# Kernel tuning notes

Hardware: AMD Instinct MI355X
Metric: run time of the kernel (lower is better)

## Reference

```python
import jax, jax.numpy as jnp
import numpy as np

D_MODEL = 1024
K_QUERY = 32
K_TOPK = 4

def setup_inputs() -> dict:
    key = jax.random.key(0)
    k1, k2, k3, k4, k5 = jax.random.split(key, 5)
    x = jax.random.normal(k1, (4, 2048, D_MODEL), dtype=jnp.float32)
    # nn.Linear(d_model, k_query): weight [k_query, d_model], bias [k_query]
    sc = 1.0 / np.sqrt(D_MODEL)
    Wq = jax.random.uniform(k2, (K_QUERY, D_MODEL), jnp.float32, -sc, sc)
    bq = jax.random.uniform(k3, (K_QUERY,), jnp.float32, -sc, sc)
    Wk = jax.random.uniform(k4, (K_QUERY, D_MODEL), jnp.float32, -sc, sc)
    bk = jax.random.uniform(k5, (K_QUERY,), jnp.float32, -sc, sc)
    return {"x": x, "Wq": Wq, "bq": bq, "Wk": Wk, "bk": bk}

def reference(x, Wq, bq, Wk, bk):
    # x: [B, T, D]
    queries = jnp.einsum('btd,kd->btk', x, Wq) + bq      # [B, T, Kq]
    keys = jnp.einsum('btd,kd->btk', x, Wk) + bk         # [B, T, Kq]
    sim = jnp.einsum('btk,bsk->bts', queries, keys)      # [B, T, T]
    sim = sim / jnp.sqrt(jnp.float32(queries.shape[-1]))
    _, topk_idx = jax.lax.top_k(sim, K_TOPK)              # [B, T, K]
    # gather neighbors per (b, t): x[b, topk_idx[b, t]] -> [B, T, K, D]
    neighbors = jax.vmap(lambda xb, ib: xb[ib])(x, topk_idx)
    gathered = neighbors.mean(axis=2)                     # [B, T, D]
    return gathered
```

## Files before the change

kernel.cpp:

```cpp
#include <hip/hip_runtime.h>
#include <math.h>

#define D_MODEL 1024
#define T_SEQ   2048
#define NBATCH  4
#define NROWS   (NBATCH * T_SEQ)
#define NOUT    64

#define XLD   1036
#define XLDH  1032

#define T16F   1024
#define T16DM  1025
#define T16DN  1281

typedef double v4df __attribute__((ext_vector_type(4)));
typedef float  v4f  __attribute__((ext_vector_type(4)));
typedef _Float16 v8hf __attribute__((ext_vector_type(8)));

__device__ __forceinline__ bool key_gt(float av, int ai, float bv, int bi) {
    return (av > bv) || (av == bv && ai < bi);
}

__device__ __forceinline__ void cmpswap(float& v0, int& i0, float& v1, int& i1) {
    bool sw = key_gt(v1, i1, v0, i0);
    float nv0 = sw ? v1 : v0, nv1 = sw ? v0 : v1;
    int   ni0 = sw ? i1 : i0, ni1 = sw ? i0 : i1;
    v0 = nv0; v1 = nv1; i0 = ni0; i1 = ni1;
}

__device__ __forceinline__ void merge4(float (&a)[4], int (&ai)[4],
                                       float b0, int j0, float b1, int j1,
                                       float b2, int j2, float b3, int j3) {
    if (!key_gt(a[0], ai[0], b3, j3)) { a[0] = b3; ai[0] = j3; }
    if (!key_gt(a[1], ai[1], b2, j2)) { a[1] = b2; ai[1] = j2; }
    if (!key_gt(a[2], ai[2], b1, j1)) { a[2] = b1; ai[2] = j1; }
    if (!key_gt(a[3], ai[3], b0, j0)) { a[3] = b0; ai[3] = j0; }
    cmpswap(a[0], ai[0], a[2], ai[2]);
    cmpswap(a[1], ai[1], a[3], ai[3]);
    cmpswap(a[0], ai[0], a[1], ai[1]);
    cmpswap(a[2], ai[2], a[3], ai[3]);
}

__device__ __forceinline__ void insert4(float (&tv)[4], int (&tix)[4], float v, int idx) {
    if (v > tv[3]) {
        bool g0 = v > tv[0], g1 = v > tv[1], g2 = v > tv[2];
        float n0 = g0 ? v : tv[0];
        int   m0 = g0 ? idx : tix[0];
        float n1 = g1 ? (g0 ? tv[0] : v) : tv[1];
        int   m1 = g1 ? (g0 ? tix[0] : idx) : tix[1];
        float n2 = g2 ? (g1 ? tv[1] : v) : tv[2];
        int   m2 = g2 ? (g1 ? tix[1] : idx) : tix[2];
        float n3 = g2 ? tv[2] : v;
        int   m3 = g2 ? tix[2] : idx;
        tv[0] = n0; tv[1] = n1; tv[2] = n2; tv[3] = n3;
        tix[0] = m0; tix[1] = m1; tix[2] = m2; tix[3] = m3;
    }
}

__device__ void run_probe(int tid, int* __restrict__ tab)
{
    __shared__ double Aref[16][4];
    __shared__ double Bref[4][16];
    __shared__ double Dref[16][16];

    const int lane = tid;
    if (tid < 64) {
        const int m = lane & 15, k = lane >> 4;
        Aref[m][k] = (double)(1 + m * 4 + k);
        Bref[k][m] = (double)(1 + k * 16 + m);
    }
    __syncthreads();
    {
        const int e = tid;
        const int m = e >> 4, n = e & 15;
        double s = 0.0;
        for (int k = 0; k < 4; ++k) s += Aref[m][k] * Bref[k][n];
        Dref[m][n] = s;
    }
    __syncthreads();

    if (tid >= 64) return;

    int found = -1;
    for (int h = 0; h < 16; ++h) {
        if (found >= 0) break;
        const int fa = h & 1, fb = (h >> 1) & 1, fd = h >> 2;
        const int am = fa ? (lane >> 2) : (lane & 15);
        const int ak = fa ? (lane & 3)  : (lane >> 4);
        const int bn = fb ? (lane >> 2) : (lane & 15);
        const int bk = fb ? (lane & 3)  : (lane >> 4);
        v4df c = {0.0, 0.0, 0.0, 0.0};
        c = __builtin_amdgcn_mfma_f64_16x16x4f64(Aref[am][ak], Bref[bk][bn], c, 0, 0, 0);
        bool ok = true;
        #pragma unroll
        for (int i = 0; i < 4; ++i) {
            int dm, dn;
            if (fd == 0)      { dm = 4 * (lane >> 4) + i; dn = lane & 15; }
            else if (fd == 1) { dn = 4 * (lane >> 4) + i; dm = lane & 15; }
            else if (fd == 2) { dm = (lane >> 4) + 4 * i; dn = lane & 15; }
            else              { dn = (lane >> 4) + 4 * i; dm = lane & 15; }
            if (c[i] != Dref[dm][dn]) ok = false;
        }
        if (__all(ok)) found = h;
    }

    const int fa = (found >= 0) ? (found & 1) : 0;
    const int fb = (found >= 0) ? ((found >> 1) & 1) : 0;
    const int fd = (found >= 0) ? (found >> 2) : 0;
    tab[1   + lane] = fa ? (lane >> 2) : (lane & 15);
    tab[65  + lane] = fa ? (lane & 3)  : (lane >> 4);
    tab[129 + lane] = fb ? (lane & 3)  : (lane >> 4);
    tab[193 + lane] = fb ? (lane >> 2) : (lane & 15);
    #pragma unroll
    for (int i = 0; i < 4; ++i) {
        int dm, dn;
        if (fd == 0)      { dm = 4 * (lane >> 4) + i; dn = lane & 15; }
        else if (fd == 1) { dn = 4 * (lane >> 4) + i; dm = lane & 15; }
        else if (fd == 2) { dm = (lane >> 4) + 4 * i; dn = lane & 15; }
        else              { dn = (lane >> 4) + 4 * i; dm = lane & 15; }
        tab[257 + lane * 4 + i] = dm;
        tab[513 + lane * 4 + i] = dn;
    }
    if (lane == 0) tab[0] = found;
}

__device__ void run_probe16(int tid, int* __restrict__ tab)
{
    __shared__ _Float16 A16[16][32];
    __shared__ _Float16 B16[32][16];
    __shared__ float    D16[16][16];

    for (int e = tid; e < 512; e += 256) {
        const int m = e >> 5, k = e & 31;
        A16[m][k] = (_Float16)(float)(1 + (3 * m + 5 * k) % 61);
        const int kk = e >> 4, n = e & 15;
        B16[kk][n] = (_Float16)(float)(1 + (7 * kk + 11 * n) % 59);
    }
    __syncthreads();
    {
        const int m = tid >> 4, n = tid & 15;
        float s = 0.f;
        for (int k = 0; k < 32; ++k) s += (float)A16[m][k] * (float)B16[k][n];
        D16[m][n] = s;
    }
    __syncthreads();

    if (tid >= 64) return;
    const int lane = tid;

    v8hf a, b;
    const int ab = (lane >> 4) * 8;
    #pragma unroll
    for (int j = 0; j < 8; ++j) {
        a[j] = A16[lane & 15][ab + j];
        b[j] = B16[ab + j][lane & 15];
    }
    v4f c = {0.f, 0.f, 0.f, 0.f};
    c = __builtin_amdgcn_mfma_f32_16x16x32_f16(a, b, c, 0, 0, 0);

    bool ok0 = true, ok1 = true;
    #pragma unroll
    for (int i = 0; i < 4; ++i) {
        ok0 = ok0 && (c[i] == D16[4 * (lane >> 4) + i][lane & 15]);
        ok1 = ok1 && (c[i] == D16[lane & 15][4 * (lane >> 4) + i]);
    }
    int found = __all(ok0) ? 0 : (__all(ok1) ? 1 : -1);
    const int fd = (found == 1) ? 1 : 0;
    #pragma unroll
    for (int i = 0; i < 4; ++i) {
        const int dm = fd ? (lane & 15) : (4 * (lane >> 4) + i);
        const int dn = fd ? (4 * (lane >> 4) + i) : (lane & 15);
        tab[T16DM + lane * 4 + i] = dm;
        tab[T16DN + lane * 4 + i] = dn;
    }
    if (lane == 0) tab[T16F] = found;
}

__global__ __launch_bounds__(256) void wprep_probe(
    const float* __restrict__ Wq, const float* __restrict__ Wk,
    double* __restrict__ Wdt, _Float16* __restrict__ Wh, _Float16* __restrict__ Wl,
    int* __restrict__ tab)
{
    const int tid = threadIdx.x;
    const int idx = blockIdx.x * 256 + tid;

    {
        const int o = idx & 63;
        const int d = idx >> 6;
        float v = (o < 32) ? Wq[(size_t)o * D_MODEL + d]
                           : Wk[(size_t)(o - 32) * D_MODEL + d];
        Wdt[(size_t)d * 64 + o] = (double)v;
    }
    {
        const int o = idx >> 10;
        const int d = idx & 1023;
        float v = (o < 32) ? Wq[(size_t)o * D_MODEL + d]
                           : Wk[(size_t)(o - 32) * D_MODEL + d];
        _Float16 h = (_Float16)v;
        Wh[(size_t)o * D_MODEL + d] = h;
        Wl[(size_t)o * D_MODEL + d] = (_Float16)(v - (float)h);
    }

    if (blockIdx.x == 0) {
        run_probe(tid, tab);
        run_probe16(tid, tab);
    }
}

__global__ __launch_bounds__(256) void proj(
    const float* __restrict__ x, const double* __restrict__ Wdt,
    const _Float16* __restrict__ Wh, const _Float16* __restrict__ Wl,
    const float* __restrict__ bq, const float* __restrict__ bk_,
    const int* __restrict__ tab,
    float* __restrict__ Qt, float* __restrict__ Kt)
{
    __shared__ __align__(16) char ldsraw[16 * XLD * 4];

    const int tid  = threadIdx.x;
    const int lane = tid & 63;
    const int wav  = tid >> 6;
    const int og   = __builtin_amdgcn_readfirstlane(wav);
    const int row0 = blockIdx.x * 16;

    const int flag16 = tab[T16F];

    if (flag16 >= 0) {
        _Float16* xh = (_Float16*)ldsraw;
        _Float16* xl = xh + 16 * XLDH;

        #pragma unroll
        for (int j = 0; j < 16; ++j) {
            const int f  = j * 256 + tid;
            const int r  = f >> 8;
            const int c4 = f & 255;
            float4 v = *reinterpret_cast<const float4*>(
                x + (size_t)(row0 + r) * D_MODEL + c4 * 4);
            union { _Float16 h[4]; short4 s; } uh, ul;
            const float vv[4] = {v.x, v.y, v.z, v.w};
            #pragma unroll
            for (int e = 0; e < 4; ++e) {
                _Float16 h = (_Float16)vv[e];
                uh.h[e] = h;
                ul.h[e] = (_Float16)(vv[e] - (float)h);
            }
            *reinterpret_cast<short4*>(&xh[r * XLDH + c4 * 4]) = uh.s;
            *reinterpret_cast<short4*>(&xl[r * XLDH + c4 * 4]) = ul.s;
        }
        __syncthreads();

        const int am   = lane & 15;
        const int koff = (lane >> 4) * 8;
        const _Float16* bhrow = Wh + (size_t)(og * 16 + am) * D_MODEL + koff;
        const _Float16* blrow = Wl + (size_t)(og * 16 + am) * D_MODEL + koff;
        const _Float16* arow  = &xh[am * XLDH + koff];
        const _Float16* arl   = &xl[am * XLDH + koff];

        v4f hh = {0.f, 0.f, 0.f, 0.f};
        v4f hl = {0.f, 0.f, 0.f, 0.f};
        v4f lh = {0.f, 0.f, 0.f, 0.f};
        #pragma unroll 8
        for (int kc = 0; kc < 32; ++kc) {
            v8hf ah = *reinterpret_cast<const v8hf*>(arow + kc * 32);
            v8hf al = *reinterpret_cast<const v8hf*>(arl  + kc * 32);
            v8hf bh = *reinterpret_cast<const v8hf*>(bhrow + kc * 32);
            v8hf bl = *reinterpret_cast<const v8hf*>(blrow + kc * 32);
            hh = __builtin_amdgcn_mfma_f32_16x16x32_f16(ah, bh, hh, 0, 0, 0);
            hl = __builtin_amdgcn_mfma_f32_16x16x32_f16(ah, bl, hl, 0, 0, 0);
            lh = __builtin_amdgcn_mfma_f32_16x16x32_f16(al, bh, lh, 0, 0, 0);
        }

        #pragma unroll
        for (int i = 0; i < 4; ++i) {
            const float tot = (hh[i] + hl[i]) + lh[i];
            const int dmv = tab[T16DM + lane * 4 + i];
            const int dnv = tab[T16DN + lane * 4 + i];
            const int out = og * 16 + dnv;
            const int row = row0 + dmv;
            const int bb  = row >> 11, t = row & 2047;
            const float bias = (out < 32) ? bq[out] : bk_[out - 32];
            const float v = tot + bias;
            if (out < 32) Qt[((size_t)bb * 32 + out) * T_SEQ + t] = v;
            else          Kt[((size_t)bb * 32 + (out - 32)) * T_SEQ + t] = v;
        }
        return;
    }

    float* xlds = (float*)ldsraw;
    #pragma unroll
    for (int j = 0; j < 16; ++j) {
        const int f  = j * 256 + tid;
        const int r  = f >> 8;
        const int c4 = f & 255;
        float4 v = *reinterpret_cast<const float4*>(
            x + (size_t)(row0 + r) * D_MODEL + c4 * 4);
        *reinterpret_cast<float4*>(&xlds[r * XLD + c4 * 4]) = v;
    }
    __syncthreads();

    const int flag = tab[0];
    v4df acc = {0.0, 0.0, 0.0, 0.0};

    if (flag >= 0) {
        const int am  = tab[1   + lane];
        const int ak  = tab[65  + lane];
        const int bkk = tab[129 + lane];
        const int bn  = tab[193 + lane];
        const double* wcol = Wdt + og * 16;
        #pragma unroll 8
        for (int kk = 0; kk < 256; ++kk) {
            double a = (double)xlds[am * XLD + kk * 4 + ak];
            double b = wcol[(size_t)(kk * 4 + bkk) * 64 + bn];
            acc = __builtin_amdgcn_mfma_f64_16x16x4f64(a, b, acc, 0, 0, 0);
        }
        #pragma unroll
        for (int i = 0; i < 4; ++i) {
            const int dmv = tab[257 + lane * 4 + i];
            const int dnv = tab[513 + lane * 4 + i];
            const int out = og * 16 + dnv;
            const int row = row0 + dmv;
            const int bb  = row >> 11, t = row & 2047;
            const double bias = (out < 32) ? (double)bq[out] : (double)bk_[out - 32];
            const float v = (float)(acc[i] + bias);
            if (out < 32) Qt[((size_t)bb * 32 + out) * T_SEQ + t] = v;
            else          Kt[((size_t)bb * 32 + (out - 32)) * T_SEQ + t] = v;
        }
    } else {
        const int n  = lane & 15;
        const int r4 = (lane >> 4) * 4;
        const int out = og * 16 + n;
        const double* wcol = Wdt + out;
        for (int d = 0; d < D_MODEL; ++d) {
            double wv = wcol[(size_t)d * 64];
            #pragma unroll
            for (int i = 0; i < 4; ++i)
                acc[i] = fma((double)xlds[(r4 + i) * XLD + d], wv, acc[i]);
        }
        #pragma unroll
        for (int i = 0; i < 4; ++i) {
            const int row = row0 + r4 + i;
            const int bb  = row >> 11, t = row & 2047;
            const double bias = (out < 32) ? (double)bq[out] : (double)bk_[out - 32];
            const float v = (float)(acc[i] + bias);
            if (out < 32) Qt[((size_t)bb * 32 + out) * T_SEQ + t] = v;
            else          Kt[((size_t)bb * 32 + (out - 32)) * T_SEQ + t] = v;
        }
    }
}

__global__ __launch_bounds__(256) void sim_topk_gather(
    const float* __restrict__ x,
    const float* __restrict__ Qt, const float* __restrict__ Kt,
    float* __restrict__ out)
{
    __shared__ float cV[4][8][4];
    __shared__ int   cI[4][8][4];
    __shared__ int   topIdx[8][4];

    const int tid  = threadIdx.x;
    const int lane = tid & 63;
    const int wav  = tid >> 6;
    const int tt   = blockIdx.x & 255;
    const int b    = blockIdx.x >> 8;
    const int tblk = tt * 8;
    const int tg   = tid & 1;
    const int sg   = tid >> 1;

    const float* QtB = Qt + (size_t)b * 32 * T_SEQ;
    const float* KtB = Kt + (size_t)b * 32 * T_SEQ;
    const int trow0 = tblk + tg * 4;

    float tv[4][4]; int tix[4][4];
    #pragma unroll
    for (int r = 0; r < 4; ++r)
        #pragma unroll
        for (int j = 0; j < 4; ++j) { tv[r][j] = -INFINITY; tix[r][j] = 0x7fffffff; }

    #pragma unroll
    for (int sweep = 0; sweep < 2; ++sweep) {
        #pragma unroll
        for (int half = 0; half < 2; ++half) {
            const int sb = sweep * 1024 + sg * 8 + half * 4;

            float acc[4][4];
            #pragma unroll
            for (int r = 0; r < 4; ++r)
                #pragma unroll
                for (int c = 0; c < 4; ++c) acc[r][c] = 0.f;

            #pragma unroll 8
            for (int i = 0; i < 32; ++i) {
                float4 qv = *reinterpret_cast<const float4*>(QtB + (size_t)i * T_SEQ + trow0);
                float4 kv = *reinterpret_cast<const float4*>(KtB + (size_t)i * T_SEQ + sb);
                const float qa[4] = {qv.x, qv.y, qv.z, qv.w};
                const float ka[4] = {kv.x, kv.y, kv.z, kv.w};
                #pragma unroll
                for (int r = 0; r < 4; ++r)
                    #pragma unroll
                    for (int c = 0; c < 4; ++c)
                        acc[r][c] = fmaf(qa[r], ka[c], acc[r][c]);
            }

            #pragma unroll
            for (int c = 0; c < 4; ++c)
                #pragma unroll
                for (int r = 0; r < 4; ++r)
                    insert4(tv[r], tix[r], acc[r][c], sb + c);
        }
    }

    #pragma unroll
    for (int m = 2; m <= 32; m <<= 1) {
        #pragma unroll
        for (int r = 0; r < 4; ++r) {
            float b0 = __shfl_xor(tv[r][0], m, 64);
            float b1 = __shfl_xor(tv[r][1], m, 64);
            float b2 = __shfl_xor(tv[r][2], m, 64);
            float b3 = __shfl_xor(tv[r][3], m, 64);
            int   j0 = __shfl_xor(tix[r][0], m, 64);
            int   j1 = __shfl_xor(tix[r][1], m, 64);
            int   j2 = __shfl_xor(tix[r][2], m, 64);
            int   j3 = __shfl_xor(tix[r][3], m, 64);
            merge4(tv[r], tix[r], b0, j0, b1, j1, b2, j2, b3, j3);
        }
    }

    if (lane < 2) {
        #pragma unroll
        for (int r = 0; r < 4; ++r)
            #pragma unroll
            for (int j = 0; j < 4; ++j) {
                cV[wav][lane * 4 + r][j] = tv[r][j];
                cI[wav][lane * 4 + r][j] = tix[r][j];
            }
    }
    __syncthreads();

    if (tid < 8) {
        float mv[4]; int mi[4];
        #pragma unroll
        for (int j = 0; j < 4; ++j) { mv[j] = cV[0][tid][j]; mi[j] = cI[0][tid][j]; }
        #pragma unroll
        for (int w = 1; w < 4; ++w)
            merge4(mv, mi,
                   cV[w][tid][0], cI[w][tid][0],
                   cV[w][tid][1], cI[w][tid][1],
                   cV[w][tid][2], cI[w][tid][2],
                   cV[w][tid][3], cI[w][tid][3]);
        #pragma unroll
        for (int j = 0; j < 4; ++j) topIdx[tid][j] = mi[j];
    }
    __syncthreads();

    const float* xb = x + (size_t)b * T_SEQ * D_MODEL;
    float* ob = out + ((size_t)b * T_SEQ + tblk) * D_MODEL;
    #pragma unroll 4
    for (int r = 0; r < 8; ++r) {
        const int i0 = topIdx[r][0], i1 = topIdx[r][1], i2 = topIdx[r][2], i3 = topIdx[r][3];
        float4 a0 = *(reinterpret_cast<const float4*>(xb + (size_t)i0 * D_MODEL) + tid);
        float4 a1 = *(reinterpret_cast<const float4*>(xb + (size_t)i1 * D_MODEL) + tid);
        float4 a2 = *(reinterpret_cast<const float4*>(xb + (size_t)i2 * D_MODEL) + tid);
        float4 a3 = *(reinterpret_cast<const float4*>(xb + (size_t)i3 * D_MODEL) + tid);
        float4 o;
        o.x = (a0.x + a1.x + a2.x + a3.x) * 0.25f;
        o.y = (a0.y + a1.y + a2.y + a3.y) * 0.25f;
        o.z = (a0.z + a1.z + a2.z + a3.z) * 0.25f;
        o.w = (a0.w + a1.w + a2.w + a3.w) * 0.25f;
        *(reinterpret_cast<float4*>(ob + (size_t)r * D_MODEL) + tid) = o;
    }
}

extern "C" void kernel_launch(void* const* d_in, const int* in_sizes, int n_in,
                              void* d_out, int out_size, void* d_ws, size_t ws_size,
                              hipStream_t stream) {
    const float* x  = (const float*)d_in[0];
    const float* Wq = (const float*)d_in[1];
    const float* bq = (const float*)d_in[2];
    const float* Wk = (const float*)d_in[3];
    const float* bk = (const float*)d_in[4];
    float* out = (float*)d_out;

    char* wsb = (char*)d_ws;
    int*      tab = (int*)wsb;
    double*   Wdt = (double*)(wsb + 8192);
    _Float16* Wh  = (_Float16*)(wsb + 8192 + 524288);
    _Float16* Wl  = (_Float16*)(wsb + 8192 + 524288 + 131072);
    float*    Qt  = (float*)(wsb + 8192 + 524288 + 262144);
    float*    Kt  = Qt + (size_t)NBATCH * 32 * T_SEQ;

    wprep_probe<<<dim3(256), dim3(256), 0, stream>>>(Wq, Wk, Wdt, Wh, Wl, tab);
    proj<<<dim3(NROWS / 16), dim3(256), 0, stream>>>(x, Wdt, Wh, Wl, bq, bk, tab, Qt, Kt);
    sim_topk_gather<<<dim3(1024), dim3(256), 0, stream>>>(x, Qt, Kt, out);
}
```

Before: 164.7 us.

## Compute similarity with split-fp16 MFMA and row-major Q/K hi/lo buffers

The projection kernel now writes Q and K as row-major fp16 hi/lo pairs instead of transposed fp32. The similarity+top-k kernel then computes the 2048x2048 scores per batch with four 16x16x32 fp16 MFMAs per tile, replacing the scalar FMA loop. Blocks cover 16 query rows instead of 8, so the grid is halved. The fp16 path is used only when the probe finds the expected MFMA layout; otherwise a new scalar fallback runs. Split-fp16 accuracy may reorder near-tied top-k neighbours.

Result: faster. 152.1 us (-7.6%).

```diff
diff --git a/kernel.cpp b/kernel.cpp
--- a/kernel.cpp
+++ b/kernel.cpp
@@ -11,8 +11,6 @@
 #define XLDH  1032
 
 #define T16F   1024
-#define T16DM  1025
-#define T16DN  1281
 
 typedef double v4df __attribute__((ext_vector_type(4)));
 typedef float  v4f  __attribute__((ext_vector_type(4)));
@@ -166,14 +164,6 @@
         ok1 = ok1 && (c[i] == D16[lane & 15][4 * (lane >> 4) + i]);
     }
     int found = __all(ok0) ? 0 : (__all(ok1) ? 1 : -1);
-    const int fd = (found == 1) ? 1 : 0;
-    #pragma unroll
-    for (int i = 0; i < 4; ++i) {
-        const int dm = fd ? (lane & 15) : (4 * (lane >> 4) + i);
-        const int dn = fd ? (4 * (lane >> 4) + i) : (lane & 15);
-        tab[T16DM + lane * 4 + i] = dm;
-        tab[T16DN + lane * 4 + i] = dn;
-    }
     if (lane == 0) tab[T16F] = found;
 }
 
@@ -213,7 +203,9 @@
     const _Float16* __restrict__ Wh, const _Float16* __restrict__ Wl,
     const float* __restrict__ bq, const float* __restrict__ bk_,
     const int* __restrict__ tab,
-    float* __restrict__ Qt, float* __restrict__ Kt)
+    float* __restrict__ Qt, float* __restrict__ Kt,
+    _Float16* __restrict__ Qh, _Float16* __restrict__ Ql,
+    _Float16* __restrict__ Kh, _Float16* __restrict__ Kl)
 {
     __shared__ __align__(16) char ldsraw[16 * XLD * 4];
 
@@ -225,7 +217,7 @@
 
     const int flag16 = tab[T16F];
 
-    if (flag16 >= 0) {
+    if (flag16 == 0) {
         _Float16* xh = (_Float16*)ldsraw;
         _Float16* xl = xh + 16 * XLDH;
 
@@ -273,15 +265,21 @@
         #pragma unroll
         for (int i = 0; i < 4; ++i) {
             const float tot = (hh[i] + hl[i]) + lh[i];
-            const int dmv = tab[T16DM + lane * 4 + i];
-            const int dnv = tab[T16DN + lane * 4 + i];
-            const int out = og * 16 + dnv;
+            const int dmv = 4 * (lane >> 4) + i;
+            const int dnv = lane & 15;
+            const int o   = og * 16 + dnv;
             const int row = row0 + dmv;
-            const int bb  = row >> 11, t = row & 2047;
-            const float bias = (out < 32) ? bq[out] : bk_[out - 32];
+            const float bias = (o < 32) ? bq[o] : bk_[o - 32];
             const float v = tot + bias;
-            if (out < 32) Qt[((size_t)bb * 32 + out) * T_SEQ + t] = v;
-            else          Kt[((size_t)bb * 32 + (out - 32)) * T_SEQ + t] = v;
+            const _Float16 h = (_Float16)v;
+            const _Float16 l = (_Float16)(v - (float)h);
+            if (o < 32) {
+                Qh[(size_t)row * 32 + o] = h;
+                Ql[(size_t)row * 32 + o] = l;
+            } else {
+                Kh[(size_t)row * 32 + (o - 32)] = h;
+                Kl[(size_t)row * 32 + (o - 32)] = l;
+            }
         }
         return;
     }
@@ -317,19 +315,19 @@
         for (int i = 0; i < 4; ++i) {
             const int dmv = tab[257 + lane * 4 + i];
             const int dnv = tab[513 + lane * 4 + i];
-            const int out = og * 16 + dnv;
+            const int o   = og * 16 + dnv;
             const int row = row0 + dmv;
             const int bb  = row >> 11, t = row & 2047;
-            const double bias = (out < 32) ? (double)bq[out] : (double)bk_[out - 32];
+            const double bias = (o < 32) ? (double)bq[o] : (double)bk_[o - 32];
             const float v = (float)(acc[i] + bias);
-            if (out < 32) Qt[((size_t)bb * 32 + out) * T_SEQ + t] = v;
-            else          Kt[((size_t)bb * 32 + (out - 32)) * T_SEQ + t] = v;
+            if (o < 32) Qt[((size_t)bb * 32 + o) * T_SEQ + t] = v;
+            else        Kt[((size_t)bb * 32 + (o - 32)) * T_SEQ + t] = v;
         }
     } else {
         const int n  = lane & 15;
         const int r4 = (lane >> 4) * 4;
-        const int out = og * 16 + n;
-        const double* wcol = Wdt + out;
+        const int o  = og * 16 + n;
+        const double* wcol = Wdt + o;
         for (int d = 0; d < D_MODEL; ++d) {
             double wv = wcol[(size_t)d * 64];
             #pragma unroll
@@ -340,122 +338,150 @@
         for (int i = 0; i < 4; ++i) {
             const int row = row0 + r4 + i;
             const int bb  = row >> 11, t = row & 2047;
-            const double bias = (out < 32) ? (double)bq[out] : (double)bk_[out - 32];
+            const double bias = (o < 32) ? (double)bq[o] : (double)bk_[o - 32];
             const float v = (float)(acc[i] + bias);
-            if (out < 32) Qt[((size_t)bb * 32 + out) * T_SEQ + t] = v;
-            else          Kt[((size_t)bb * 32 + (out - 32)) * T_SEQ + t] = v;
+            if (o < 32) Qt[((size_t)bb * 32 + o) * T_SEQ + t] = v;
+            else        Kt[((size_t)bb * 32 + (o - 32)) * T_SEQ + t] = v;
         }
     }
 }
 
 __global__ __launch_bounds__(256) void sim_topk_gather(
     const float* __restrict__ x,
+    const _Float16* __restrict__ Qh, const _Float16* __restrict__ Ql,
+    const _Float16* __restrict__ Kh, const _Float16* __restrict__ Kl,
     const float* __restrict__ Qt, const float* __restrict__ Kt,
+    const int* __restrict__ tab,
     float* __restrict__ out)
 {
-    __shared__ float cV[4][8][4];
-    __shared__ int   cI[4][8][4];
-    __shared__ int   topIdx[8][4];
+    __shared__ float sV[16][16][4];
+    __shared__ int   sI[16][16][4];
+    __shared__ int   topIdx[16][4];
 
     const int tid  = threadIdx.x;
     const int lane = tid & 63;
     const int wav  = tid >> 6;
-    const int tt   = blockIdx.x & 255;
-    const int b    = blockIdx.x >> 8;
-    const int tblk = tt * 8;
-    const int tg   = tid & 1;
-    const int sg   = tid >> 1;
-
-    const float* QtB = Qt + (size_t)b * 32 * T_SEQ;
-    const float* KtB = Kt + (size_t)b * 32 * T_SEQ;
-    const int trow0 = tblk + tg * 4;
-
-    float tv[4][4]; int tix[4][4];
-    #pragma unroll
-    for (int r = 0; r < 4; ++r)
-        #pragma unroll
-        for (int j = 0; j < 4; ++j) { tv[r][j] = -INFINITY; tix[r][j] = 0x7fffffff; }
-
-    #pragma unroll
-    for (int sweep = 0; sweep < 2; ++sweep) {
-        #pragma unroll
-        for (int half = 0; half < 2; ++half) {
-            const int sb = sweep * 1024 + sg * 8 + half * 4;
-
-            float acc[4][4];
+    const int tt   = blockIdx.x & 127;
+    const int b    = blockIdx.x >> 7;
+    const int row0g = b * T_SEQ + tt * 16;
+
+    if (tab[T16F] == 0) {
+        const int m  = lane & 15;
+        const int ko = (lane >> 4) * 8;
+        v8hf ah = *reinterpret_cast<const v8hf*>(Qh + (size_t)(row0g + m) * 32 + ko);
+        v8hf al = *reinterpret_cast<const v8hf*>(Ql + (size_t)(row0g + m) * 32 + ko);
+        const _Float16* KhB = Kh + (size_t)b * T_SEQ * 32;
+        const _Float16* KlB = Kl + (size_t)b * T_SEQ * 32;
+
+        float tv[4][4]; int tix[4][4];
+        #pragma unroll
+        for (int r = 0; r < 4; ++r)
+            #pragma unroll
+            for (int j = 0; j < 4; ++j) { tv[r][j] = -INFINITY; tix[r][j] = 0x7fffffff; }
+
+        const int sq = wav * 512;
+        #pragma unroll 4
+        for (int st = 0; st < 32; ++st) {
+            const int s0 = sq + st * 16;
+            v8hf bh = *reinterpret_cast<const v8hf*>(KhB + (size_t)(s0 + m) * 32 + ko);
+            v8hf bl = *reinterpret_cast<const v8hf*>(KlB + (size_t)(s0 + m) * 32 + ko);
+            v4f c = {0.f, 0.f, 0.f, 0.f};
+            c = __builtin_amdgcn_mfma_f32_16x16x32_f16(ah, bh, c, 0, 0, 0);
+            c = __builtin_amdgcn_mfma_f32_16x16x32_f16(ah, bl, c, 0, 0, 0);
+            c = __builtin_amdgcn_mfma_f32_16x16x32_f16(al, bh, c, 0, 0, 0);
+            c = __builtin_amdgcn_mfma_f32_16x16x32_f16(al, bl, c, 0, 0, 0);
+            const int col = s0 + m;
+            #pragma unroll
+            for (int i = 0; i < 4; ++i) insert4(tv[i], tix[i], c[i], col);
+        }
+
+        #pragma unroll
+        for (int mk = 1; mk <= 8; mk <<= 1) {
+            #pragma unroll
+            for (int r = 0; r < 4; ++r) {
+                float b0 = __shfl_xor(tv[r][0], mk, 64);
+                float b1 = __shfl_xor(tv[r][1], mk, 64);
+                float b2 = __shfl_xor(tv[r][2], mk, 64);
+                float b3 = __shfl_xor(tv[r][3], mk, 64);
+                int   j0 = __shfl_xor(tix[r][0], mk, 64);
+                int   j1 = __shfl_xor(tix[r][1], mk, 64);
+                int   j2 = __shfl_xor(tix[r][2], mk, 64);
+                int   j3 = __shfl_xor(tix[r][3], mk, 64);
+                merge4(tv[r], tix[r], b0, j0, b1, j1, b2, j2, b3, j3);
+            }
+        }
+
+        if ((lane & 15) == 0) {
+            const int rbase = (lane >> 4) * 4;
             #pragma unroll
             for (int r = 0; r < 4; ++r)
                 #pragma unroll
-                for (int c = 0; c < 4; ++c) acc[r][c] = 0.f;
-
+                for (int j = 0; j < 4; ++j) {
+                    sV[wav][rbase + r][j] = tv[r][j];
+                    sI[wav][rbase + r][j] = tix[r][j];
+                }
+        }
+        __syncthreads();
+
+        if (tid < 16) {
+            float mv[4]; int mi[4];
+            #pragma unroll
+            for (int j = 0; j < 4; ++j) { mv[j] = sV[0][tid][j]; mi[j] = sI[0][tid][j]; }
+            #pragma unroll
+            for (int w = 1; w < 4; ++w)
+                merge4(mv, mi,
+                       sV[w][tid][0], sI[w][tid][0],
+                       sV[w][tid][1], sI[w][tid][1],
+                       sV[w][tid][2], sI[w][tid][2],
+                       sV[w][tid][3], sI[w][tid][3]);
+            #pragma unroll
+            for (int j = 0; j < 4; ++j) topIdx[tid][j] = mi[j];
+        }
+        __syncthreads();
+    } else {
+        const float* QtB = Qt + (size_t)b * 32 * T_SEQ;
+        const float* KtB = Kt + (size_t)b * 32 * T_SEQ;
+        const int row   = tid >> 4;
+        const int chunk = tid & 15;
+        const int trow  = tt * 16 + row;
+        float q[32];
+        #pragma unroll 8
+        for (int i = 0; i < 32; ++i) q[i] = QtB[(size_t)i * T_SEQ + trow];
+        float tv4[4]; int tix4[4];
+        #pragma unroll
+        for (int j = 0; j < 4; ++j) { tv4[j] = -INFINITY; tix4[j] = 0x7fffffff; }
+        const int sbeg = chunk * 128;
+        for (int s = sbeg; s < sbeg + 128; ++s) {
+            float sum = 0.f;
             #pragma unroll 8
-            for (int i = 0; i < 32; ++i) {
-                float4 qv = *reinterpret_cast<const float4*>(QtB + (size_t)i * T_SEQ + trow0);
-                float4 kv = *reinterpret_cast<const float4*>(KtB + (size_t)i * T_SEQ + sb);
-                const float qa[4] = {qv.x, qv.y, qv.z, qv.w};
-                const float ka[4] = {kv.x, kv.y, kv.z, kv.w};
-                #pragma unroll
-                for (int r = 0; r < 4; ++r)
-                    #pragma unroll
-                    for (int c = 0; c < 4; ++c)
-                        acc[r][c] = fmaf(qa[r], ka[c], acc[r][c]);
-            }
-
-            #pragma unroll
-            for (int c = 0; c < 4; ++c)
-                #pragma unroll
-                for (int r = 0; r < 4; ++r)
-                    insert4(tv[r], tix[r], acc[r][c], sb + c);
-        }
-    }
-
-    #pragma unroll
-    for (int m = 2; m <= 32; m <<= 1) {
-        #pragma unroll
-        for (int r = 0; r < 4; ++r) {
-            float b0 = __shfl_xor(tv[r][0], m, 64);
-            float b1 = __shfl_xor(tv[r][1], m, 64);
-            float b2 = __shfl_xor(tv[r][2], m, 64);
-            float b3 = __shfl_xor(tv[r][3], m, 64);
-            int   j0 = __shfl_xor(tix[r][0], m, 64);
-            int   j1 = __shfl_xor(tix[r][1], m, 64);
-            int   j2 = __shfl_xor(tix[r][2], m, 64);
-            int   j3 = __shfl_xor(tix[r][3], m, 64);
-            merge4(tv[r], tix[r], b0, j0, b1, j1, b2, j2, b3, j3);
-        }
-    }
-
-    if (lane < 2) {
-        #pragma unroll
-        for (int r = 0; r < 4; ++r)
-            #pragma unroll
-            for (int j = 0; j < 4; ++j) {
-                cV[wav][lane * 4 + r][j] = tv[r][j];
-                cI[wav][lane * 4 + r][j] = tix[r][j];
-            }
-    }
-    __syncthreads();
-
-    if (tid < 8) {
-        float mv[4]; int mi[4];
-        #pragma unroll
-        for (int j = 0; j < 4; ++j) { mv[j] = cV[0][tid][j]; mi[j] = cI[0][tid][j]; }
-        #pragma unroll
-        for (int w = 1; w < 4; ++w)
-            merge4(mv, mi,
-                   cV[w][tid][0], cI[w][tid][0],
-                   cV[w][tid][1], cI[w][tid][1],
-                   cV[w][tid][2], cI[w][tid][2],
-                   cV[w][tid][3], cI[w][tid][3]);
-        #pragma unroll
-        for (int j = 0; j < 4; ++j) topIdx[tid][j] = mi[j];
-    }
-    __syncthreads();
+            for (int i = 0; i < 32; ++i)
+                sum = fmaf(q[i], KtB[(size_t)i * T_SEQ + s], sum);
+            insert4(tv4, tix4, sum, s);
+        }
+        #pragma unroll
+        for (int j = 0; j < 4; ++j) { sV[row][chunk][j] = tv4[j]; sI[row][chunk][j] = tix4[j]; }
+        __syncthreads();
+        if (tid < 16) {
+            float mv[4]; int mi[4];
+            #pragma unroll
+            for (int j = 0; j < 4; ++j) { mv[j] = sV[tid][0][j]; mi[j] = sI[tid][0][j]; }
+            #pragma unroll
+            for (int cc = 1; cc < 16; ++cc)
+                merge4(mv, mi,
+                       sV[tid][cc][0], sI[tid][cc][0],
+                       sV[tid][cc][1], sI[tid][cc][1],
+                       sV[tid][cc][2], sI[tid][cc][2],
+                       sV[tid][cc][3], sI[tid][cc][3]);
+            #pragma unroll
+            for (int j = 0; j < 4; ++j) topIdx[tid][j] = mi[j];
+        }
+        __syncthreads();
+    }
 
     const float* xb = x + (size_t)b * T_SEQ * D_MODEL;
-    float* ob = out + ((size_t)b * T_SEQ + tblk) * D_MODEL;
-    #pragma unroll 4
-    for (int r = 0; r < 8; ++r) {
+    float* ob = out + (size_t)row0g * D_MODEL;
+    #pragma unroll 2
+    for (int r = 0; r < 16; ++r) {
         const int i0 = topIdx[r][0], i1 = topIdx[r][1], i2 = topIdx[r][2], i3 = topIdx[r][3];
         float4 a0 = *(reinterpret_cast<const float4*>(xb + (size_t)i0 * D_MODEL) + tid);
         float4 a1 = *(reinterpret_cast<const float4*>(xb + (size_t)i1 * D_MODEL) + tid);
@@ -487,8 +513,13 @@
     _Float16* Wl  = (_Float16*)(wsb + 8192 + 524288 + 131072);
     float*    Qt  = (float*)(wsb + 8192 + 524288 + 262144);
     float*    Kt  = Qt + (size_t)NBATCH * 32 * T_SEQ;
+    _Float16* Qh  = (_Float16*)((char*)Kt + (size_t)NBATCH * 32 * T_SEQ * 4);
+    _Float16* Ql  = Qh + (size_t)NROWS * 32;
+    _Float16* Kh  = Ql + (size_t)NROWS * 32;
+    _Float16* Kl  = Kh + (size_t)NROWS * 32;
 
     wprep_probe<<<dim3(256), dim3(256), 0, stream>>>(Wq, Wk, Wdt, Wh, Wl, tab);
-    proj<<<dim3(NROWS / 16), dim3(256), 0, stream>>>(x, Wdt, Wh, Wl, bq, bk, tab, Qt, Kt);
-    sim_topk_gather<<<dim3(1024), dim3(256), 0, stream>>>(x, Qt, Kt, out);
-}
+    proj<<<dim3(NROWS / 16), dim3(256), 0, stream>>>(x, Wdt, Wh, Wl, bq, bk, tab,
+                                                     Qt, Kt, Qh, Ql, Kh, Kl);
+    sim_topk_gather<<<dim3(512), dim3(256), 0, stream>>>(x, Qh, Ql, Kh, Kl, Qt, Kt, tab, out);
+}
```
